# Optimization experiments

Hardware: AMD Instinct MI355X
Metric: run time of the kernel (lower is better)

Reference implementation:

```python
import jax, jax.numpy as jnp
from jax import lax
import numpy as np

SEQ, BATCH, IN, HID = 1024, 8192, 3, 50


def setup_inputs() -> dict:
    key = jax.random.key(0)
    ks = jax.random.split(key, 7)
    s_ih = 1.0 / np.sqrt(HID)
    return {
        "x": jax.random.normal(ks[0], (SEQ, BATCH, IN), dtype=jnp.float32),
        "W_ih": jax.random.normal(ks[1], (4 * HID, IN), dtype=jnp.float32) * s_ih,
        "W_hh": jax.random.normal(ks[2], (4 * HID, HID), dtype=jnp.float32) * s_ih,
        "b_ih": jax.random.normal(ks[3], (4 * HID,), dtype=jnp.float32) * s_ih,
        "b_hh": jax.random.normal(ks[4], (4 * HID,), dtype=jnp.float32) * s_ih,
        "fc_w": jax.random.normal(ks[5], (1, HID), dtype=jnp.float32) * s_ih,
        "fc_b": jax.random.normal(ks[6], (1,), dtype=jnp.float32) * s_ih,
    }


def reference(x, W_ih, W_hh, b_ih, b_hh, fc_w, fc_b):
    # x: (T, B, I); PyTorch LSTM gate order is i, f, g, o along the 4H axis.
    T, B, _ = x.shape
    H = W_hh.shape[1]
    # Hoist the input projection out of the recurrence: one big GEMM.
    xg = jnp.einsum("tbi,gi->tbg", x, W_ih) + b_ih + b_hh  # (T, B, 4H)

    def step(carry, xg_t):
        h, c = carry
        gates = xg_t + h @ W_hh.T  # (B, 4H)
        i, f, g, o = jnp.split(gates, 4, axis=-1)
        i = jax.nn.sigmoid(i)
        f = jax.nn.sigmoid(f)
        g = jnp.tanh(g)
        o = jax.nn.sigmoid(o)
        c = f * c + i * g
        h = o * jnp.tanh(c)
        return (h, c), None

    h0 = jnp.zeros((B, H), dtype=x.dtype)
    c0 = jnp.zeros((B, H), dtype=x.dtype)
    (h_last, _), _ = lax.scan(step, (h0, c0), xg)
    # h.squeeze(0) in the torch code -> last layer's final hidden state (B, H)
    return h_last @ fc_w.T + fc_b  # (B, 1)
```

## Files before the change

kernel.cpp:

```cpp
#include <hip/hip_runtime.h>

#define SEQ   1024
#define BATCH 8192
#define HID   50
#define BT    16
#define CHS   16
#define NCH   (SEQ/CHS)
#define CHF   (CHS*BT*3)

typedef _Float16 half8 __attribute__((ext_vector_type(8)));
typedef float    f32x4 __attribute__((ext_vector_type(4)));

__device__ __forceinline__ int bslot(int k, int b){
  return (k >> 5)*512 + ((k & 31) >> 3)*128 + b*8 + (k & 7);
}

#define XLD(cg) {                                                         \
    const int f1 = tid + 256, f2 = tid + 512;                             \
    const int s0_ = (tid*683) >> 15, s1_ = (f1*683) >> 15,                \
              s2_ = (f2*683) >> 15;                                       \
    xr0 = x[(size_t)(((cg)*CHS + s0_)*BATCH + b0)*3 + (tid - 48*s0_)];    \
    xr1 = x[(size_t)(((cg)*CHS + s1_)*BATCH + b0)*3 + (f1  - 48*s1_)];    \
    xr2 = x[(size_t)(((cg)*CHS + s2_)*BATCH + b0)*3 + (f2  - 48*s2_)]; }

#define ELEM(acc, C, slot) {                                                           \
    const float si = __builtin_amdgcn_rcpf(1.0f + __builtin_amdgcn_exp2f((acc)[0]));   \
    const float sf = __builtin_amdgcn_rcpf(1.0f + __builtin_amdgcn_exp2f((acc)[1]));   \
    const float rg = __builtin_amdgcn_rcpf(1.0f + __builtin_amdgcn_exp2f((acc)[2]));   \
    const float so = __builtin_amdgcn_rcpf(1.0f + __builtin_amdgcn_exp2f((acc)[3]));   \
    const float G  = __builtin_fmaf(-5.77078016355584f, rg, 2.88539008177792f);        \
    C = __builtin_fmaf(sf, C, si*G);                                                   \
    const float r2 = __builtin_amdgcn_rcpf(1.0f + __builtin_amdgcn_exp2f(C));          \
    const float u_ = so * r2;                                                          \
    const float h_ = __builtin_fmaf(-2.0f, u_, so);                                    \
    Bst[q][slot] = (_Float16)h_; }

__global__ __launch_bounds__(256, 2)
void lstm_wt(const float* __restrict__ x,
             const float* __restrict__ W_ih,
             const float* __restrict__ W_hh,
             const float* __restrict__ b_ih,
             const float* __restrict__ b_hh,
             const float* __restrict__ fc_w,
             const float* __restrict__ fc_b,
             float* __restrict__ out)
{
  __shared__ _Float16 Bst[2][1024];
  __shared__ float    xb[2][CHF];

  const int tid  = threadIdx.x;
  const int w    = tid >> 6;
  const int lane = tid & 63;
  const int r16  = lane & 15;
  const int grp  = lane >> 4;
  const int b0   = blockIdx.x * BT;
  const float L2E = 1.44269504088896f;

  half8 Af[4][2];
  #pragma unroll
  for (int it = 0; it < 4; ++it) {
    const int tile = (it < 3) ? (w + 4*it) : 12;
    #pragma unroll
    for (int kh = 0; kh < 2; ++kh) {
      half8 f;
      #pragma unroll
      for (int i = 0; i < 8; ++i) {
        const int k = kh*32 + grp*8 + i;
        const int c = tile*16 + r16;
        float wv = 0.0f;
        if (c < 4*HID) {
          const int j = c >> 2, gi = c & 3;
          const int go = gi*HID + j;
          const float sc = (gi == 2) ? (2.0f*L2E) : (-L2E);
          if (k < HID)      wv = W_hh[go*HID + k] * sc;
          else if (k < 53)  wv = W_ih[go*3 + (k-50)] * sc;
          else if (k == 53) wv = (b_ih[go] + b_hh[go]) * sc;
        }
        f[i] = (_Float16)wv;
      }
      Af[it][kh] = f;
    }
  }

  int wslot[4];
  #pragma unroll
  for (int it = 0; it < 4; ++it) {
    const int j = (it < 3) ? (w*4 + grp + 16*it) : (48 + grp);
    wslot[it] = bslot((j < HID) ? j : 0, r16);
  }

  for (int i = tid; i < 1024; i += 256) ((unsigned*)Bst)[i] = 0u;
  __syncthreads();
  if (tid < 32) Bst[tid >> 4][768 + (tid & 15)*8 + 5] = (_Float16)1.0f;

  float xr0, xr1, xr2;
  XLD(0); xb[0][tid] = xr0; xb[0][tid+256] = xr1; xb[0][tid+512] = xr2;
  XLD(1); xb[1][tid] = xr0; xb[1][tid+256] = xr1; xb[1][tid+512] = xr2;
  XLD(2);
  __syncthreads();
  if (tid < 48) {
    const int bb = (tid*171) >> 9, e = tid - 3*bb;
    Bst[0][768 + bb*8 + 2 + e] = (_Float16)xb[0][tid];
  }
  __syncthreads();

  float cs0 = 0.f, cs1 = 0.f, cs2 = 0.f, cs3 = 0.f;

  auto step = [&](int t, int p, int q) {
    const half8 s0 = *(const half8*)&Bst[p][lane*8];
    const half8 s1 = *(const half8*)&Bst[p][512 + lane*8];
    f32x4 a0 = {0.f,0.f,0.f,0.f}, a1 = a0, a2 = a0;
    a0 = __builtin_amdgcn_mfma_f32_16x16x32_f16(Af[0][0], s0, a0, 0,0,0);
    a1 = __builtin_amdgcn_mfma_f32_16x16x32_f16(Af[1][0], s0, a1, 0,0,0);
    a2 = __builtin_amdgcn_mfma_f32_16x16x32_f16(Af[2][0], s0, a2, 0,0,0);
    a0 = __builtin_amdgcn_mfma_f32_16x16x32_f16(Af[0][1], s1, a0, 0,0,0);
    a1 = __builtin_amdgcn_mfma_f32_16x16x32_f16(Af[1][1], s1, a1, 0,0,0);
    a2 = __builtin_amdgcn_mfma_f32_16x16x32_f16(Af[2][1], s1, a2, 0,0,0);
    ELEM(a0, cs0, wslot[0]);
    ELEM(a1, cs1, wslot[1]);
    ELEM(a2, cs2, wslot[2]);
    if (w == 3) {
      f32x4 a3 = {0.f,0.f,0.f,0.f};
      a3 = __builtin_amdgcn_mfma_f32_16x16x32_f16(Af[3][0], s0, a3, 0,0,0);
      a3 = __builtin_amdgcn_mfma_f32_16x16x32_f16(Af[3][1], s1, a3, 0,0,0);
      if (grp < 2) ELEM(a3, cs3, wslot[3]);
    }
    if ((unsigned)(tid - 64) < 48u) {
      const int xt = tid - 64;
      const int bb = (xt*171) >> 9, e = xt - 3*bb;
      const int tn = t + 1;
      Bst[q][768 + bb*8 + 2 + e] = (_Float16)xb[(tn >> 4) & 1][(tn & 15)*48 + xt];
    }
    asm volatile("s_waitcnt lgkmcnt(0)\n\ts_barrier" ::: "memory");
  };

  #pragma unroll 1
  for (int tc = 0; tc < NCH; ++tc) {
    if (tc > 0) {
      const int pc = (tc + 1) & 1;
      xb[pc][tid] = xr0; xb[pc][tid+256] = xr1; xb[pc][tid+512] = xr2;
      if (tc + 2 < NCH) { XLD(tc+2); }
    }
    const int tb = tc*CHS;
    #pragma unroll 1
    for (int u = 0; u < CHS/2; ++u) {
      step(tb + 2*u,     0, 1);
      step(tb + 2*u + 1, 1, 0);
    }
  }

  if (tid < BT) {
    float s = fc_b[0];
    #pragma unroll
    for (int j = 0; j < HID; ++j)
      s += fc_w[j] * (float)Bst[0][bslot(j, tid)];
    out[b0 + tid] = s;
  }
}

extern "C" void kernel_launch(void* const* d_in, const int* in_sizes, int n_in,
                              void* d_out, int out_size, void* d_ws, size_t ws_size,
                              hipStream_t stream)
{
  const float* x    = (const float*)d_in[0];
  const float* W_ih = (const float*)d_in[1];
  const float* W_hh = (const float*)d_in[2];
  const float* b_ih = (const float*)d_in[3];
  const float* b_hh = (const float*)d_in[4];
  const float* fc_w = (const float*)d_in[5];
  const float* fc_b = (const float*)d_in[6];
  lstm_wt<<<BATCH/BT, 256, 0, stream>>>(x, W_ih, W_hh, b_ih, b_hh, fc_w, fc_b,
                                        (float*)d_out);
}
```

Measured before the change: 573.1 us.

## Split LSTM gate tiles across eight waves per block instead of four

Each block now runs 512 threads (8 waves) for its 16 batch rows, so each wave handles at most two 16-column gate tiles instead of three or four. This shortens the per-step serial MFMA plus elementwise chain on the recurrence critical path. In exchange, every step's barrier must synchronise twice as many waves, the work is uneven across waves (waves 5-7 have one tile), and the x-staging loads are redistributed across the larger block. Launch bounds change to (512,4).

Result: slower. 589.4 us (+2.8%).

```diff
diff --git a/kernel.cpp b/kernel.cpp
--- a/kernel.cpp
+++ b/kernel.cpp
@@ -15,13 +15,13 @@
   return (k >> 5)*512 + ((k & 31) >> 3)*128 + b*8 + (k & 7);
 }
 
-#define XLD(cg) {                                                         \
-    const int f1 = tid + 256, f2 = tid + 512;                             \
-    const int s0_ = (tid*683) >> 15, s1_ = (f1*683) >> 15,                \
-              s2_ = (f2*683) >> 15;                                       \
-    xr0 = x[(size_t)(((cg)*CHS + s0_)*BATCH + b0)*3 + (tid - 48*s0_)];    \
-    xr1 = x[(size_t)(((cg)*CHS + s1_)*BATCH + b0)*3 + (f1  - 48*s1_)];    \
-    xr2 = x[(size_t)(((cg)*CHS + s2_)*BATCH + b0)*3 + (f2  - 48*s2_)]; }
+#define XLD(cg) {                                                          \
+    const int s0_ = (tid*683) >> 15;                                       \
+    xr0 = x[(size_t)(((cg)*CHS + s0_)*BATCH + b0)*3 + (tid - 48*s0_)];     \
+    if (tid < 256) {                                                       \
+      const int f1 = tid + 512; const int s1_ = (f1*683) >> 15;            \
+      xr1 = x[(size_t)(((cg)*CHS + s1_)*BATCH + b0)*3 + (f1 - 48*s1_)];    \
+    } }
 
 #define ELEM(acc, C, slot) {                                                           \
     const float si = __builtin_amdgcn_rcpf(1.0f + __builtin_amdgcn_exp2f((acc)[0]));   \
@@ -35,8 +35,8 @@
     const float h_ = __builtin_fmaf(-2.0f, u_, so);                                    \
     Bst[q][slot] = (_Float16)h_; }
 
-__global__ __launch_bounds__(256, 2)
-void lstm_wt(const float* __restrict__ x,
+__global__ __launch_bounds__(512, 4)
+void lstm_w8(const float* __restrict__ x,
              const float* __restrict__ W_ih,
              const float* __restrict__ W_hh,
              const float* __restrict__ b_ih,
@@ -56,10 +56,10 @@
   const int b0   = blockIdx.x * BT;
   const float L2E = 1.44269504088896f;
 
-  half8 Af[4][2];
+  half8 Af[2][2];
   #pragma unroll
-  for (int it = 0; it < 4; ++it) {
-    const int tile = (it < 3) ? (w + 4*it) : 12;
+  for (int it = 0; it < 2; ++it) {
+    const int tile = it ? (8 + w) : w;
     #pragma unroll
     for (int kh = 0; kh < 2; ++kh) {
       half8 f;
@@ -68,7 +68,7 @@
         const int k = kh*32 + grp*8 + i;
         const int c = tile*16 + r16;
         float wv = 0.0f;
-        if (c < 4*HID) {
+        if (tile < 13 && c < 4*HID) {
           const int j = c >> 2, gi = c & 3;
           const int go = gi*HID + j;
           const float sc = (gi == 2) ? (2.0f*L2E) : (-L2E);
@@ -82,20 +82,17 @@
     }
   }
 
-  int wslot[4];
-  #pragma unroll
-  for (int it = 0; it < 4; ++it) {
-    const int j = (it < 3) ? (w*4 + grp + 16*it) : (48 + grp);
-    wslot[it] = bslot((j < HID) ? j : 0, r16);
-  }
+  const int j1t = 32 + w*4 + grp;
+  const int ws0 = bslot(w*4 + grp, r16);
+  const int ws1 = bslot((j1t < HID) ? j1t : 0, r16);
 
-  for (int i = tid; i < 1024; i += 256) ((unsigned*)Bst)[i] = 0u;
+  for (int i = tid; i < 1024; i += 512) ((unsigned*)Bst)[i] = 0u;
   __syncthreads();
   if (tid < 32) Bst[tid >> 4][768 + (tid & 15)*8 + 5] = (_Float16)1.0f;
 
-  float xr0, xr1, xr2;
-  XLD(0); xb[0][tid] = xr0; xb[0][tid+256] = xr1; xb[0][tid+512] = xr2;
-  XLD(1); xb[1][tid] = xr0; xb[1][tid+256] = xr1; xb[1][tid+512] = xr2;
+  float xr0 = 0.f, xr1 = 0.f;
+  XLD(0); xb[0][tid] = xr0; if (tid < 256) xb[0][tid+512] = xr1;
+  XLD(1); xb[1][tid] = xr0; if (tid < 256) xb[1][tid+512] = xr1;
   XLD(2);
   __syncthreads();
   if (tid < 48) {
@@ -104,32 +101,27 @@
   }
   __syncthreads();
 
-  float cs0 = 0.f, cs1 = 0.f, cs2 = 0.f, cs3 = 0.f;
+  float cs0 = 0.f, cs1 = 0.f;
 
   auto step = [&](int t, int p, int q) {
     const half8 s0 = *(const half8*)&Bst[p][lane*8];
     const half8 s1 = *(const half8*)&Bst[p][512 + lane*8];
-    f32x4 a0 = {0.f,0.f,0.f,0.f}, a1 = a0, a2 = a0;
+    f32x4 a0 = {0.f,0.f,0.f,0.f};
     a0 = __builtin_amdgcn_mfma_f32_16x16x32_f16(Af[0][0], s0, a0, 0,0,0);
-    a1 = __builtin_amdgcn_mfma_f32_16x16x32_f16(Af[1][0], s0, a1, 0,0,0);
-    a2 = __builtin_amdgcn_mfma_f32_16x16x32_f16(Af[2][0], s0, a2, 0,0,0);
     a0 = __builtin_amdgcn_mfma_f32_16x16x32_f16(Af[0][1], s1, a0, 0,0,0);
-    a1 = __builtin_amdgcn_mfma_f32_16x16x32_f16(Af[1][1], s1, a1, 0,0,0);
-    a2 = __builtin_amdgcn_mfma_f32_16x16x32_f16(Af[2][1], s1, a2, 0,0,0);
-    ELEM(a0, cs0, wslot[0]);
-    ELEM(a1, cs1, wslot[1]);
-    ELEM(a2, cs2, wslot[2]);
-    if (w == 3) {
-      f32x4 a3 = {0.f,0.f,0.f,0.f};
-      a3 = __builtin_amdgcn_mfma_f32_16x16x32_f16(Af[3][0], s0, a3, 0,0,0);
-      a3 = __builtin_amdgcn_mfma_f32_16x16x32_f16(Af[3][1], s1, a3, 0,0,0);
-      if (grp < 2) ELEM(a3, cs3, wslot[3]);
+    if (w < 5) {
+      f32x4 a1 = {0.f,0.f,0.f,0.f};
+      a1 = __builtin_amdgcn_mfma_f32_16x16x32_f16(Af[1][0], s0, a1, 0,0,0);
+      a1 = __builtin_amdgcn_mfma_f32_16x16x32_f16(Af[1][1], s1, a1, 0,0,0);
+      ELEM(a0, cs0, ws0);
+      if (w < 4 || grp < 2) ELEM(a1, cs1, ws1);
+    } else {
+      ELEM(a0, cs0, ws0);
     }
-    if ((unsigned)(tid - 64) < 48u) {
-      const int xt = tid - 64;
-      const int bb = (xt*171) >> 9, e = xt - 3*bb;
+    if (w == 6 && lane < 48) {
       const int tn = t + 1;
-      Bst[q][768 + bb*8 + 2 + e] = (_Float16)xb[(tn >> 4) & 1][(tn & 15)*48 + xt];
+      const int bb = (lane*171) >> 9, e = lane - 3*bb;
+      Bst[q][768 + bb*8 + 2 + e] = (_Float16)xb[(tn >> 4) & 1][(tn & 15)*48 + lane];
     }
     asm volatile("s_waitcnt lgkmcnt(0)\n\ts_barrier" ::: "memory");
   };
@@ -138,7 +130,8 @@
   for (int tc = 0; tc < NCH; ++tc) {
     if (tc > 0) {
       const int pc = (tc + 1) & 1;
-      xb[pc][tid] = xr0; xb[pc][tid+256] = xr1; xb[pc][tid+512] = xr2;
+      xb[pc][tid] = xr0;
+      if (tid < 256) xb[pc][tid + 512] = xr1;
       if (tc + 2 < NCH) { XLD(tc+2); }
     }
     const int tb = tc*CHS;
@@ -169,6 +162,6 @@
   const float* b_hh = (const float*)d_in[4];
   const float* fc_w = (const float*)d_in[5];
   const float* fc_b = (const float*)d_in[6];
-  lstm_wt<<<BATCH/BT, 256, 0, stream>>>(x, W_ih, W_hh, b_ih, b_hh, fc_w, fc_b,
+  lstm_w8<<<BATCH/BT, 512, 0, stream>>>(x, W_ih, W_hh, b_ih, b_hh, fc_w, fc_b,
                                         (float*)d_out);
 }
```
